# Optimization experiments

Hardware: AMD Instinct MI355X
Metric: run time of the kernel (lower is better)

## Reference

```python
import jax, jax.numpy as jnp
import numpy as np

E = 64          # moe_num_experts
H = 1024        # hidden_size
F = 2816        # per_expert_ff_dim
T = 4096        # total tokens (equal split: 64 per expert)


def setup_inputs() -> dict:
    key = jax.random.key(0)
    k1, k2, k3, k4 = jax.random.split(key, 4)
    s = 1.0 / np.sqrt(H)
    return {
        "x": jax.random.normal(k1, (T, H), dtype=jnp.float32),
        "tokens_per_expert": jnp.full((E,), T // E, dtype=jnp.int32),
        "w1": jax.random.normal(k2, (E * F, H), dtype=jnp.float32) * s,
        "w3": jax.random.normal(k3, (E * F, H), dtype=jnp.float32) * s,
        "w2": jax.random.normal(k4, (E * F, H), dtype=jnp.float32) * s,
    }


def reference(x, tokens_per_expert, w1, w3, w2):
    # Tokens are grouped contiguously per expert with an equal split,
    # so the variable-size grouped GEMM (gg.ops.gmm) reduces to a batched einsum.
    tpe = x.shape[0] // E
    xg = x.reshape(E, tpe, H)            # [E, t, h]
    w1e = w1.reshape(E, F, H)
    w3e = w3.reshape(E, F, H)
    w2e = w2.reshape(E, F, H)
    # gmm(x, w1, trans_b=True): per-expert x @ w1[e].T
    h1 = jnp.einsum("eth,efh->etf", xg, w1e)   # [E, t, f]
    h3 = jnp.einsum("eth,efh->etf", xg, w3e)   # [E, t, f]
    gated = jax.nn.silu(h1) * h3               # SwiGLU
    # gmm(gated, w2): per-expert gated @ w2[e]  ([t,f] @ [f,h])
    out = jnp.einsum("etf,efh->eth", gated, w2e)
    return out.reshape(-1, H)
```

## Files before the change

kernel.cpp:

```cpp
#include <hip/hip_runtime.h>
#include <hip/hip_bf16.h>

#define NE   64
#define NH   1024
#define NF   2816
#define TPE  64
#define PITCH 72

typedef __attribute__((ext_vector_type(8))) short bf16x8;
typedef __attribute__((ext_vector_type(4))) float f32x4;

__device__ __forceinline__ ushort f2bf(float f) {
    union { float f; unsigned u; } v; v.f = f;
    unsigned r = v.u + 0x7fffu + ((v.u >> 16) & 1u);
    return (ushort)(r >> 16);
}

__device__ __forceinline__ float bf2f(ushort u) {
    union { unsigned u; float f; } v; v.u = ((unsigned)u) << 16;
    return v.f;
}

__device__ __forceinline__ bf16x8 cvt8(f32x4 lo, f32x4 hi) {
    bf16x8 r;
    #pragma unroll
    for (int j = 0; j < 4; ++j) {
        r[j]     = (short)f2bf(lo[j]);
        r[4 + j] = (short)f2bf(hi[j]);
    }
    return r;
}

__global__ __launch_bounds__(256)
void xcast(const float* __restrict__ x, ushort* __restrict__ xb) {
    const int i = blockIdx.x * 256 + threadIdx.x;
    const f32x4 a = *(const f32x4*)(x + (size_t)i * 8);
    const f32x4 b = *(const f32x4*)(x + (size_t)i * 8 + 4);
    *(bf16x8*)(xb + (size_t)i * 8) = cvt8(a, b);
}

template <int GATE>
__global__ __launch_bounds__(256, 2)
void k1_mm(const ushort* __restrict__ xb,
           const float* __restrict__ w,
           const ushort* __restrict__ h1in,
           ushort* __restrict__ outp) {
    __shared__ ushort lW[64 * PITCH];

    const int jt   = blockIdx.x;
    const int e    = blockIdx.y;
    const int tid  = threadIdx.x;
    const int lane = tid & 63;
    const int wid  = tid >> 6;
    const int m15  = lane & 15;
    const int hi   = lane >> 4;
    const int mrow = wid * 16 + m15;

    const ushort* xA = xb + ((size_t)e * TPE + mrow) * NH;
    const float*  B  = w  + ((size_t)e * NF + (size_t)jt * 64) * NH;

    f32x4 acc[4];
    #pragma unroll
    for (int nf = 0; nf < 4; ++nf) acc[nf] = f32x4{0.f, 0.f, 0.f, 0.f};

    const int srow = tid >> 4;
    const int sc4  = (tid & 15) * 4;

    for (int kt = 0; kt < NH / 64; ++kt) {
        const size_t kb = (size_t)kt * 64;
        __syncthreads();
        #pragma unroll
        for (int r = 0; r < 4; ++r) {
            const int row = srow + r * 16;
            const float4 v = *(const float4*)(B + (size_t)row * NH + kb + sc4);
            ushort4 u;
            u.x = f2bf(v.x); u.y = f2bf(v.y); u.z = f2bf(v.z); u.w = f2bf(v.w);
            *(ushort4*)(&lW[row * PITCH + sc4]) = u;
        }
        __syncthreads();

        #pragma unroll
        for (int ks = 0; ks < 2; ++ks) {
            const int koff = ks * 32 + hi * 8;
            const bf16x8 af = *(const bf16x8*)(xA + kb + koff);
            #pragma unroll
            for (int nf = 0; nf < 4; ++nf) {
                const bf16x8 bw = *(const bf16x8*)(&lW[(nf * 16 + m15) * PITCH + koff]);
                acc[nf] = __builtin_amdgcn_mfma_f32_16x16x32_bf16(af, bw, acc[nf], 0, 0, 0);
            }
        }
    }

    #pragma unroll
    for (int nf = 0; nf < 4; ++nf) {
        #pragma unroll
        for (int i = 0; i < 4; ++i) {
            const int row = wid * 16 + hi * 4 + i;
            const int col = jt * 64 + nf * 16 + m15;
            const size_t idx = ((size_t)e * TPE + row) * NF + col;
            if (GATE) {
                const float h1v = bf2f(h1in[idx]);
                const float h3v = acc[nf][i];
                const float s   = (h1v / (1.f + __expf(-h1v))) * h3v;
                outp[idx] = f2bf(s);
            } else {
                outp[idx] = f2bf(acc[nf][i]);
            }
        }
    }
}

__global__ __launch_bounds__(256, 2)
void k2_down(const ushort* __restrict__ g,
             const float* __restrict__ w2,
             float* __restrict__ out) {
    __shared__ ushort lA[64 * PITCH];
    __shared__ ushort lB[64 * PITCH];

    const int jt   = blockIdx.x;
    const int e    = blockIdx.y;
    const int tid  = threadIdx.x;
    const int lane = tid & 63;
    const int wid  = tid >> 6;

    const ushort* A = g  + (size_t)e * TPE * NF;
    const float*  B = w2 + (size_t)e * NF * NH + (size_t)jt * 64;
    float* O = out + (size_t)e * TPE * NH + (size_t)jt * 64;

    f32x4 acc[4];
    for (int nf = 0; nf < 4; ++nf) acc[nf] = f32x4{0.f, 0.f, 0.f, 0.f};

    for (int kt = 0; kt < NF / 64; ++kt) {
        __syncthreads();
        #pragma unroll
        for (int r = 0; r < 2; ++r) {
            const int q   = tid + r * 256;
            const int row = q >> 3;
            const int k8  = (q & 7) * 8;
            *(bf16x8*)(&lA[row * PITCH + k8]) =
                *(const bf16x8*)(A + (size_t)row * NF + kt * 64 + k8);
        }
        {
            const int n  = tid & 63;
            const int kq = (tid >> 6) * 4;
            #pragma unroll
            for (int r = 0; r < 4; ++r) {
                const int ks = kq + r * 16;
                const size_t base = (size_t)(kt * 64 + ks) * NH + n;
                const float f0 = B[base];
                const float f1 = B[base + NH];
                const float f2 = B[base + 2 * (size_t)NH];
                const float f3 = B[base + 3 * (size_t)NH];
                ushort4 b;
                b.x = f2bf(f0); b.y = f2bf(f1); b.z = f2bf(f2); b.w = f2bf(f3);
                *(ushort4*)(&lB[n * PITCH + ks]) = b;
            }
        }
        __syncthreads();

        const int mrow = wid * 16 + (lane & 15);
        #pragma unroll
        for (int ks = 0; ks < 2; ++ks) {
            const int koff = ks * 32 + ((lane >> 4) * 8);
            const bf16x8 af = *(const bf16x8*)(&lA[mrow * PITCH + koff]);
            #pragma unroll
            for (int nf = 0; nf < 4; ++nf) {
                const bf16x8 bfr = *(const bf16x8*)(&lB[(nf * 16 + (lane & 15)) * PITCH + koff]);
                acc[nf] = __builtin_amdgcn_mfma_f32_16x16x32_bf16(af, bfr, acc[nf], 0, 0, 0);
            }
        }
    }

    #pragma unroll
    for (int nf = 0; nf < 4; ++nf) {
        #pragma unroll
        for (int i = 0; i < 4; ++i) {
            const int row = wid * 16 + ((lane >> 4) * 4) + i;
            const int col = nf * 16 + (lane & 15);
            O[(size_t)row * NH + col] = acc[nf][i];
        }
    }
}

extern "C" void kernel_launch(void* const* d_in, const int* in_sizes, int n_in,
                              void* d_out, int out_size, void* d_ws, size_t ws_size,
                              hipStream_t stream) {
    const float* x  = (const float*)d_in[0];
    const float* w1 = (const float*)d_in[2];
    const float* w3 = (const float*)d_in[3];
    const float* w2 = (const float*)d_in[4];
    float* out = (float*)d_out;
    ushort* gated = (ushort*)d_ws;
    ushort* xbf   = (ushort*)((char*)d_ws + (32u << 20));
    ushort* h1    = (ushort*)((char*)d_ws + (48u << 20));

    xcast<<<dim3((TPE * NE * NH) / (256 * 8)), dim3(256), 0, stream>>>(x, xbf);

    dim3 g1(NF / 64, NE);
    k1_mm<0><<<g1, dim3(256), 0, stream>>>(xbf, w1, nullptr, h1);
    k1_mm<1><<<g1, dim3(256), 0, stream>>>(xbf, w3, h1, gated);

    dim3 g2(NH / 64, NE);
    k2_down<<<g2, dim3(256), 0, stream>>>(gated, w2, out);
}
```

Baseline: 504.6 us.

## Restructure up-projection to stream full-K 16-row weight tiles per block

The up-projection kernel now gives each block 176 output features, handled as 11 sequential tiles of 16 weight rows. Each tile loads the full K=1024 extent into shared memory with contiguous row reads, in place of the earlier 64x64 K-step tiles. The grid shrinks from 44 to 16 blocks per expert and launch bounds ask for 4 blocks per SM. The aim is more coalesced weight streaming and fewer tiny tiles. In exchange each tile needs 32 serial MFMAs on one accumulator, and there are fewer blocks in flight.

```diff
diff --git a/kernel.cpp b/kernel.cpp
--- a/kernel.cpp
+++ b/kernel.cpp
@@ -6,6 +6,7 @@
 #define NF   2816
 #define TPE  64
 #define PITCH 72
+#define WP   1032
 
 typedef __attribute__((ext_vector_type(8))) short bf16x8;
 typedef __attribute__((ext_vector_type(4))) float f32x4;
@@ -40,71 +41,61 @@
 }
 
 template <int GATE>
-__global__ __launch_bounds__(256, 2)
+__global__ __launch_bounds__(256, 4)
 void k1_mm(const ushort* __restrict__ xb,
            const float* __restrict__ w,
            const ushort* __restrict__ h1in,
            ushort* __restrict__ outp) {
-    __shared__ ushort lW[64 * PITCH];
+    __shared__ ushort lW[16 * WP];
 
-    const int jt   = blockIdx.x;
+    const int jtg  = blockIdx.x;
     const int e    = blockIdx.y;
     const int tid  = threadIdx.x;
     const int lane = tid & 63;
     const int wid  = tid >> 6;
     const int m15  = lane & 15;
     const int hi   = lane >> 4;
-    const int mrow = wid * 16 + m15;
 
-    const ushort* xA = xb + ((size_t)e * TPE + mrow) * NH;
-    const float*  B  = w  + ((size_t)e * NF + (size_t)jt * 64) * NH;
+    const ushort* xA = xb + ((size_t)e * TPE + wid * 16 + m15) * NH;
+    const float* B = w + ((size_t)e * NF + (size_t)jtg * 176) * NH;
 
-    f32x4 acc[4];
-    #pragma unroll
-    for (int nf = 0; nf < 4; ++nf) acc[nf] = f32x4{0.f, 0.f, 0.f, 0.f};
-
-    const int srow = tid >> 4;
-    const int sc4  = (tid & 15) * 4;
-
-    for (int kt = 0; kt < NH / 64; ++kt) {
-        const size_t kb = (size_t)kt * 64;
+    for (int t = 0; t < 11; ++t) {
         __syncthreads();
         #pragma unroll
         for (int r = 0; r < 4; ++r) {
-            const int row = srow + r * 16;
-            const float4 v = *(const float4*)(B + (size_t)row * NH + kb + sc4);
-            ushort4 u;
-            u.x = f2bf(v.x); u.y = f2bf(v.y); u.z = f2bf(v.z); u.w = f2bf(v.w);
-            *(ushort4*)(&lW[row * PITCH + sc4]) = u;
+            const int row = wid * 4 + r;
+            const float* src = B + ((size_t)(t * 16 + row)) * NH;
+            #pragma unroll
+            for (int i = 0; i < 4; ++i) {
+                const float4 v = *(const float4*)(src + i * 256 + lane * 4);
+                ushort4 u;
+                u.x = f2bf(v.x); u.y = f2bf(v.y); u.z = f2bf(v.z); u.w = f2bf(v.w);
+                *(ushort4*)(&lW[row * WP + i * 256 + lane * 4]) = u;
+            }
         }
         __syncthreads();
 
-        #pragma unroll
-        for (int ks = 0; ks < 2; ++ks) {
-            const int koff = ks * 32 + hi * 8;
-            const bf16x8 af = *(const bf16x8*)(xA + kb + koff);
-            #pragma unroll
-            for (int nf = 0; nf < 4; ++nf) {
-                const bf16x8 bw = *(const bf16x8*)(&lW[(nf * 16 + m15) * PITCH + koff]);
-                acc[nf] = __builtin_amdgcn_mfma_f32_16x16x32_bf16(af, bw, acc[nf], 0, 0, 0);
-            }
+        f32x4 acc = f32x4{0.f, 0.f, 0.f, 0.f};
+        #pragma unroll 8
+        for (int kk = 0; kk < 32; ++kk) {
+            const int ko = kk * 32 + hi * 8;
+            const bf16x8 af = *(const bf16x8*)(xA + ko);
+            const bf16x8 bw = *(const bf16x8*)(&lW[m15 * WP + ko]);
+            acc = __builtin_amdgcn_mfma_f32_16x16x32_bf16(af, bw, acc, 0, 0, 0);
         }
-    }
 
-    #pragma unroll
-    for (int nf = 0; nf < 4; ++nf) {
         #pragma unroll
         for (int i = 0; i < 4; ++i) {
-            const int row = wid * 16 + hi * 4 + i;
-            const int col = jt * 64 + nf * 16 + m15;
-            const size_t idx = ((size_t)e * TPE + row) * NF + col;
+            const int token = wid * 16 + hi * 4 + i;
+            const int fcol  = jtg * 176 + t * 16 + m15;
+            const size_t idx = ((size_t)e * TPE + token) * NF + fcol;
             if (GATE) {
                 const float h1v = bf2f(h1in[idx]);
-                const float h3v = acc[nf][i];
+                const float h3v = acc[i];
                 const float s   = (h1v / (1.f + __expf(-h1v))) * h3v;
                 outp[idx] = f2bf(s);
             } else {
-                outp[idx] = f2bf(acc[nf][i]);
+                outp[idx] = f2bf(acc[i]);
             }
         }
     }
@@ -196,7 +187,7 @@
 
     xcast<<<dim3((TPE * NE * NH) / (256 * 8)), dim3(256), 0, stream>>>(x, xbf);
 
-    dim3 g1(NF / 64, NE);
+    dim3 g1(16, NE);
     k1_mm<0><<<g1, dim3(256), 0, stream>>>(xbf, w1, nullptr, h1);
     k1_mm<1><<<g1, dim3(256), 0, stream>>>(xbf, w3, h1, gated);
 
```

Measured after the change: 668.4 us. +32.5%, slower.
